# Optimization experiments

Measured on AMD Instinct MI355X. Metric: run time of the kernel, lower is better.

Reference implementation:

```python
import jax, jax.numpy as jnp
import numpy as np

C = 64
G = 4
K = 3
GC = C // G
OS = 1.0  # offset_scale
OM_DIM = int(np.ceil(G * K * K * 3 / 8) * 8)  # 112, padded; only first G*27 used


def setup_inputs() -> dict:
    key = jax.random.key(0)
    ks = jax.random.split(key, 8)
    B, H, W = 2, 384, 384
    s = 0.02
    return {
        "inp": jax.random.normal(ks[0], (B, C, H, W), jnp.float32),
        "Wv": jax.random.normal(ks[1], (C, C), jnp.float32) * s,
        "bv": jnp.zeros((C,), jnp.float32),
        "Wdw": jax.random.normal(ks[2], (C, 1, K, K), jnp.float32) * s,
        "bdw": jnp.zeros((C,), jnp.float32),
        "Wom": jax.random.normal(ks[3], (C, OM_DIM), jnp.float32) * s,
        "bom": jnp.zeros((OM_DIM,), jnp.float32),
        "Wo": jax.random.normal(ks[4], (C, C), jnp.float32) * s,
    }


def _bilinear(v, px, py, H, W, b_idx, g_idx):
    # v: (B,H,W,G,GC); px,py: (B,H,W,G) pixel coords; zero padding outside.
    x0 = jnp.floor(px)
    y0 = jnp.floor(py)
    wx1 = px - x0
    wy1 = py - y0
    x0i = x0.astype(jnp.int32)
    y0i = y0.astype(jnp.int32)
    out = jnp.zeros(px.shape + (v.shape[-1],), v.dtype)
    for dy, wy in ((0, 1.0 - wy1), (1, wy1)):
        for dx, wx in ((0, 1.0 - wx1), (1, wx1)):
            xi = x0i + dx
            yi = y0i + dy
            valid = ((xi >= 0) & (xi < W) & (yi >= 0) & (yi < H)).astype(v.dtype)
            xc = jnp.clip(xi, 0, W - 1)
            yc = jnp.clip(yi, 0, H - 1)
            g = v[b_idx, yc, xc, g_idx]  # (B,H,W,G,GC)
            out = out + g * (wy * wx * valid)[..., None]
    return out


def reference(inp, Wv, bv, Wdw, bdw, Wom, bom, Wo):
    B, _, H, W = inp.shape
    x = inp.transpose(0, 2, 3, 1)  # (B,H,W,C)
    # value projection, split into groups
    value = (x @ Wv + bv).reshape(B, H, W, G, GC)
    # depthwise conv on input feeds the offset/mask predictor
    dw = jax.lax.conv_general_dilated(
        inp, Wdw, window_strides=(1, 1), padding=[(1, 1), (1, 1)],
        feature_group_count=C) + bdw[None, :, None, None]
    om = dw.transpose(0, 2, 3, 1) @ Wom + bom  # (B,H,W,OM_DIM)
    om = om[..., : G * K * K * 3].reshape(B, H, W, G, K * K * 3)
    off = om[..., : K * K * 2].reshape(B, H, W, G, K * K, 2)  # (dx,dy) per point
    mask = om[..., K * K * 2:]  # (B,H,W,G,K*K), no softmax in DCNv4

    base_x = jnp.arange(W, dtype=value.dtype)[None, None, :, None]
    base_y = jnp.arange(H, dtype=value.dtype)[None, :, None, None]
    b_idx = jnp.arange(B)[:, None, None, None]
    g_idx = jnp.arange(G)[None, None, None, :]

    out = jnp.zeros((B, H, W, G, GC), value.dtype)
    k = 0
    for ky in range(K):
        for kx in range(K):
            dx = off[..., k, 0]
            dy = off[..., k, 1]
            px = base_x + ((kx - K // 2) + dx) * OS
            py = base_y + ((ky - K // 2) + dy) * OS
            samp = _bilinear(value, px, py, H, W, b_idx, g_idx)
            out = out + samp * mask[..., k][..., None]
            k += 1

    out = out.reshape(B, H, W, C) @ Wo  # output_proj, no bias (output_bias=False)
    return out.transpose(0, 3, 1, 2)  # back to (B,C,H,W)
```

## Files before the change

### kernel.cpp

```cpp
#include <hip/hip_runtime.h>
#include <hip/hip_bf16.h>
#include <math.h>

namespace {
constexpr int kH = 384, kW = 384, kBn = 2;
constexpr int kHW = kH * kW;
constexpr int kOMD = 112;
constexpr int kNB = kBn * (kHW / 64);
constexpr int kNB8 = kNB / 8;
}

__device__ __forceinline__ int swz(int bid) {
    return (bid & 7) * kNB8 + (bid >> 3);
}

__device__ __forceinline__ void fma4(float* acc, float a, float4 w) {
    acc[0] = fmaf(a, w.x, acc[0]);
    acc[1] = fmaf(a, w.y, acc[1]);
    acc[2] = fmaf(a, w.z, acc[2]);
    acc[3] = fmaf(a, w.w, acc[3]);
}

__device__ __forceinline__ float bl(unsigned u) {
    return __uint_as_float(u << 16);
}
__device__ __forceinline__ float bh(unsigned u) {
    return __uint_as_float(u & 0xffff0000u);
}
__device__ __forceinline__ unsigned short f2bf(float f) {
    union { __hip_bfloat16 b; unsigned short s; } u;
    u.b = __float2bfloat16(f);
    return u.s;
}

__global__ __launch_bounds__(256) void k_value(
        const float* __restrict__ inp, const float* __restrict__ Wv,
        const float* __restrict__ bv, unsigned short* __restrict__ value) {
    __shared__ float xin[64][65];
    __shared__ float wv[64 * 64];
    const int tid = threadIdx.x;
    const int bid = swz(blockIdx.x);
    const int b = bid / (kHW / 64);
    const int pix0 = (bid % (kHW / 64)) * 64;
    const float* ib = inp + (size_t)b * 64 * kHW + pix0;
    for (int i = tid; i < 4096; i += 256) {
        const int c = i >> 6, p = i & 63;
        xin[p][c] = ib[(size_t)c * kHW + p];
        wv[i] = Wv[i];
    }
    __syncthreads();
    const int tc = tid & 15, tp = tid >> 4;
    float acc[4][4];
    {
        const float4 b4 = *(const float4*)(bv + tc * 4);
        #pragma unroll
        for (int q = 0; q < 4; ++q) {
            acc[q][0] = b4.x; acc[q][1] = b4.y; acc[q][2] = b4.z; acc[q][3] = b4.w;
        }
    }
    #pragma unroll 4
    for (int ci = 0; ci < 64; ++ci) {
        const float4 w4 = *(const float4*)&wv[ci * 64 + tc * 4];
        #pragma unroll
        for (int q = 0; q < 4; ++q) {
            fma4(acc[q], xin[tp * 4 + q][ci], w4);
        }
    }
    const int g = tc >> 2, cq = tc & 3;
    #pragma unroll
    for (int q = 0; q < 4; ++q) {
        ushort4 st;
        st.x = f2bf(acc[q][0]); st.y = f2bf(acc[q][1]);
        st.z = f2bf(acc[q][2]); st.w = f2bf(acc[q][3]);
        ushort4* vo = (ushort4*)(value +
                ((size_t)(b * 4 + g) * kHW + pix0 + tp * 4 + q) * 16 + cq * 4);
        *vo = st;
    }
}

__global__ __launch_bounds__(256) void k_main(
        const float* __restrict__ inp, const float* __restrict__ Wdw,
        const float* __restrict__ bdw, const float* __restrict__ Wom,
        const float* __restrict__ bom, const float* __restrict__ Wo,
        const unsigned short* __restrict__ value, float* __restrict__ out) {
    __shared__ float lds1[64][68];

    const int tid = threadIdx.x;
    const int bid = swz(blockIdx.x);
    const int b = bid / (kH * (kW / 64));
    const int rem = bid % (kH * (kW / 64));
    const int h = rem / (kW / 64);
    const int w0 = (rem % (kW / 64)) * 64;

    const int p = tid & 63;
    const int g = tid >> 6;
    const int gs = __builtin_amdgcn_readfirstlane(g);

    {
        const int w = w0 + p;
        #pragma unroll 4
        for (int cc = 0; cc < 16; ++cc) {
            const int c = gs * 16 + cc;
            const float* ib = inp + (size_t)(b * 64 + c) * kHW;
            float s = bdw[c];
            #pragma unroll
            for (int r = 0; r < 3; ++r) {
                const int y = h - 1 + r;
                if (y >= 0 && y < kH) {
                    const float* rowp = ib + (size_t)y * kW;
                    #pragma unroll
                    for (int kx = 0; kx < 3; ++kx) {
                        const int x = w - 1 + kx;
                        const float v = (x >= 0 && x < kW) ? rowp[x] : 0.f;
                        s = fmaf(v, Wdw[c * 9 + r * 3 + kx], s);
                    }
                }
            }
            lds1[c][p] = s;
        }
    }
    __syncthreads();

    float om[27];
    {
        const float* bg = bom + gs * 27;
        #pragma unroll
        for (int j = 0; j < 27; ++j) om[j] = bg[j];
        #pragma unroll 4
        for (int ci = 0; ci < 64; ++ci) {
            const float a = lds1[ci][p];
            const float* wr = Wom + ci * kOMD + gs * 27;
            #pragma unroll
            for (int j = 0; j < 27; ++j) om[j] = fmaf(a, wr[j], om[j]);
        }
    }
    __syncthreads();

    {
        float acc[16];
        #pragma unroll
        for (int j = 0; j < 16; ++j) acc[j] = 0.f;
        const float fw = (float)(w0 + p);
        const float fh = (float)h;
        const unsigned short* vbase = value + (size_t)(b * 4 + gs) * kHW * 16;
        #pragma unroll
        for (int k = 0; k < 9; ++k) {
            const int ky = k / 3, kx = k % 3;
            const float dx = om[2 * k];
            const float dy = om[2 * k + 1];
            const float m = om[18 + k];
            const float px = fw + (float)(kx - 1) + dx;
            const float py = fh + (float)(ky - 1) + dy;
            const float x0f = floorf(px), y0f = floorf(py);
            const int x0 = (int)x0f, y0 = (int)y0f;
            const float wx1 = px - x0f, wy1 = py - y0f;
            const float wx0 = 1.f - wx1, wy0 = 1.f - wy1;
            #pragma unroll
            for (int cor = 0; cor < 4; ++cor) {
                const int dy2 = cor >> 1, dx2 = cor & 1;
                const int xi = x0 + dx2, yi = y0 + dy2;
                float wgt = (dy2 ? wy1 : wy0) * (dx2 ? wx1 : wx0) * m;
                if (xi < 0 || xi >= kW || yi < 0 || yi >= kH) wgt = 0.f;
                const int xc = min(max(xi, 0), kW - 1);
                const int yc = min(max(yi, 0), kH - 1);
                const uint4* vp = (const uint4*)(vbase +
                        ((size_t)yc * kW + xc) * 16);
                const uint4 u0 = vp[0];
                const uint4 u1 = vp[1];
                acc[0]  = fmaf(wgt, bl(u0.x), acc[0]);
                acc[1]  = fmaf(wgt, bh(u0.x), acc[1]);
                acc[2]  = fmaf(wgt, bl(u0.y), acc[2]);
                acc[3]  = fmaf(wgt, bh(u0.y), acc[3]);
                acc[4]  = fmaf(wgt, bl(u0.z), acc[4]);
                acc[5]  = fmaf(wgt, bh(u0.z), acc[5]);
                acc[6]  = fmaf(wgt, bl(u0.w), acc[6]);
                acc[7]  = fmaf(wgt, bh(u0.w), acc[7]);
                acc[8]  = fmaf(wgt, bl(u1.x), acc[8]);
                acc[9]  = fmaf(wgt, bh(u1.x), acc[9]);
                acc[10] = fmaf(wgt, bl(u1.y), acc[10]);
                acc[11] = fmaf(wgt, bh(u1.y), acc[11]);
                acc[12] = fmaf(wgt, bl(u1.z), acc[12]);
                acc[13] = fmaf(wgt, bh(u1.z), acc[13]);
                acc[14] = fmaf(wgt, bl(u1.w), acc[14]);
                acc[15] = fmaf(wgt, bh(u1.w), acc[15]);
            }
        }
        #pragma unroll
        for (int j = 0; j < 16; ++j) lds1[gs * 16 + j][p] = acc[j];
    }
    __syncthreads();

    {
        const int cg = gs;
        float acc[16];
        #pragma unroll
        for (int j = 0; j < 16; ++j) acc[j] = 0.f;
        #pragma unroll 4
        for (int ci = 0; ci < 64; ++ci) {
            const float a = lds1[ci][p];
            const float* wr = Wo + ci * 64 + cg * 16;
            #pragma unroll
            for (int j = 0; j < 16; ++j) acc[j] = fmaf(a, wr[j], acc[j]);
        }
        float* ob = out + (size_t)(b * 64 + cg * 16) * kHW + (size_t)h * kW + w0 + p;
        #pragma unroll
        for (int j = 0; j < 16; ++j) ob[(size_t)j * kHW] = acc[j];
    }
}

extern "C" void kernel_launch(void* const* d_in, const int* in_sizes, int n_in,
                              void* d_out, int out_size, void* d_ws, size_t ws_size,
                              hipStream_t stream) {
    const float* inp = (const float*)d_in[0];
    const float* Wv  = (const float*)d_in[1];
    const float* bv  = (const float*)d_in[2];
    const float* Wdw = (const float*)d_in[3];
    const float* bdw = (const float*)d_in[4];
    const float* Wom = (const float*)d_in[5];
    const float* bom = (const float*)d_in[6];
    const float* Wo  = (const float*)d_in[7];
    float* outp = (float*)d_out;
    unsigned short* value = (unsigned short*)d_ws;

    k_value<<<kNB, 256, 0, stream>>>(inp, Wv, bv, value);
    k_main<<<kNB, 256, 0, stream>>>(inp, Wdw, bdw, Wom, bom, Wo, value, outp);
}
```

Before: 328.2 us.

## Restructure value projection to per-pixel threads with uniform scalar weight loads

The value-projection kernel no longer stages Wv in shared memory. Each thread now handles one pixel and one group's 16 channels, and reads weights through wave-uniform (scalar) loads. The input tile is loaded with float4 loads into an unpadded LDS tile, and each thread writes its bf16 outputs as two 16-byte stores. This removes the weight staging and the transposed strided LDS writes, and cuts shared-memory footprint. In exchange, each thread uses more accumulator registers and issues more scalar weight loads.

```diff
diff --git a/kernel.cpp b/kernel.cpp
--- a/kernel.cpp
+++ b/kernel.cpp
@@ -36,46 +36,43 @@
 __global__ __launch_bounds__(256) void k_value(
         const float* __restrict__ inp, const float* __restrict__ Wv,
         const float* __restrict__ bv, unsigned short* __restrict__ value) {
-    __shared__ float xin[64][65];
-    __shared__ float wv[64 * 64];
+    __shared__ float xin[64][64];
     const int tid = threadIdx.x;
     const int bid = swz(blockIdx.x);
     const int b = bid / (kHW / 64);
     const int pix0 = (bid % (kHW / 64)) * 64;
     const float* ib = inp + (size_t)b * 64 * kHW + pix0;
-    for (int i = tid; i < 4096; i += 256) {
-        const int c = i >> 6, p = i & 63;
-        xin[p][c] = ib[(size_t)c * kHW + p];
-        wv[i] = Wv[i];
-    }
-    __syncthreads();
-    const int tc = tid & 15, tp = tid >> 4;
-    float acc[4][4];
-    {
-        const float4 b4 = *(const float4*)(bv + tc * 4);
-        #pragma unroll
-        for (int q = 0; q < 4; ++q) {
-            acc[q][0] = b4.x; acc[q][1] = b4.y; acc[q][2] = b4.z; acc[q][3] = b4.w;
-        }
+    for (int i = tid; i < 1024; i += 256) {
+        const int c = i >> 4, p4 = (i & 15) << 2;
+        const float4 v = *(const float4*)(ib + (size_t)c * kHW + p4);
+        *(float4*)&xin[c][p4] = v;
+    }
+    __syncthreads();
+
+    const int p = tid & 63;
+    const int g = __builtin_amdgcn_readfirstlane(tid >> 6);
+
+    float acc[16];
+    {
+        const float* bg = bv + g * 16;
+        #pragma unroll
+        for (int j = 0; j < 16; ++j) acc[j] = bg[j];
     }
     #pragma unroll 4
     for (int ci = 0; ci < 64; ++ci) {
-        const float4 w4 = *(const float4*)&wv[ci * 64 + tc * 4];
-        #pragma unroll
-        for (int q = 0; q < 4; ++q) {
-            fma4(acc[q], xin[tp * 4 + q][ci], w4);
-        }
-    }
-    const int g = tc >> 2, cq = tc & 3;
+        const float a = xin[ci][p];
+        const float* wr = Wv + ci * 64 + g * 16;
+        #pragma unroll
+        for (int j = 0; j < 16; ++j) acc[j] = fmaf(a, wr[j], acc[j]);
+    }
+
+    unsigned u[8];
     #pragma unroll
-    for (int q = 0; q < 4; ++q) {
-        ushort4 st;
-        st.x = f2bf(acc[q][0]); st.y = f2bf(acc[q][1]);
-        st.z = f2bf(acc[q][2]); st.w = f2bf(acc[q][3]);
-        ushort4* vo = (ushort4*)(value +
-                ((size_t)(b * 4 + g) * kHW + pix0 + tp * 4 + q) * 16 + cq * 4);
-        *vo = st;
-    }
+    for (int j = 0; j < 8; ++j)
+        u[j] = (unsigned)f2bf(acc[2 * j]) | ((unsigned)f2bf(acc[2 * j + 1]) << 16);
+    uint4* vo = (uint4*)(value + ((size_t)(b * 4 + g) * kHW + pix0 + p) * 16);
+    vo[0] = make_uint4(u[0], u[1], u[2], u[3]);
+    vo[1] = make_uint4(u[4], u[5], u[6], u[7]);
 }
 
 __global__ __launch_bounds__(256) void k_main(
```

New measurement: 332.5 us. Within noise of the previous version (+1.3%).
